# Optimization experiments

Hardware: AMD Instinct MI355X
Metric: run time of the kernel (lower is better)

## Reference

```python
import jax, jax.numpy as jnp
import numpy as np
from jax import lax

N_CLASS = 32000
N_HIDDEN = 512
S_ENC = 1024
S_DEC = 256


def setup_inputs() -> dict:
    key = jax.random.key(0)
    ks = jax.random.split(key, 16)
    C, H = N_CLASS, N_HIDDEN
    sC = np.float32(1.0 / np.sqrt(C))
    sH = np.float32(1.0 / np.sqrt(H))
    f32 = jnp.float32
    return {
        "encoder_inputs": jax.random.normal(ks[0], (1, S_ENC, C), f32),
        "hidden_0": jnp.zeros((1, 1, H), f32),
        "decoder_inputs": jax.random.normal(ks[1], (1, S_DEC, C), f32),
        # encoder RNN params (torch nn.RNN layout: W_ih [H,C], W_hh [H,H])
        "enc_Wih": jax.random.normal(ks[2], (H, C), f32) * sC,
        "enc_Whh": jax.random.normal(ks[3], (H, H), f32) * sH,
        "enc_bih": jax.random.normal(ks[4], (H,), f32) * sH,
        "enc_bhh": jax.random.normal(ks[5], (H,), f32) * sH,
        # decoder RNN params
        "dec_Wih": jax.random.normal(ks[6], (H, C), f32) * sC,
        "dec_Whh": jax.random.normal(ks[7], (H, H), f32) * sH,
        "dec_bih": jax.random.normal(ks[8], (H,), f32) * sH,
        "dec_bhh": jax.random.normal(ks[9], (H,), f32) * sH,
        # attention Linear [H,H]
        "attn_W": jax.random.normal(ks[10], (H, H), f32) * sH,
        "attn_b": jax.random.normal(ks[11], (H,), f32) * sH,
        # output Linear [C, 2H]
        "out_W": jax.random.normal(ks[12], (C, 2 * H), f32) * sH,
        "out_b": jax.random.normal(ks[13], (C,), f32) * sH,
    }


def _rnn_scan(x, h0, Wih, Whh, bih, bhh):
    # x: [S, C], h0: [H] -> hs: [S, H], hT: [H]  (tanh vanilla RNN)
    def step(h, xt):
        h = jnp.tanh(xt @ Wih.T + bih + h @ Whh.T + bhh)
        return h, h
    hT, hs = lax.scan(step, h0, x)
    return hs, hT


def reference(encoder_inputs, hidden_0, decoder_inputs,
              enc_Wih, enc_Whh, enc_bih, enc_bhh,
              dec_Wih, dec_Whh, dec_bih, dec_bhh,
              attn_W, attn_b, out_W, out_b):
    enc_x = encoder_inputs[0]   # [S_enc, C] (batch=1)
    dec_x = decoder_inputs[0]   # [S_dec, C]
    h0 = hidden_0[0, 0]         # [H]

    enc_hs, enc_hT = _rnn_scan(enc_x, h0, enc_Wih, enc_Whh, enc_bih, enc_bhh)

    # score_i = dot(dec_h, attn(enc_h_i)); precompute attn over all encoder states
    attn_enc = enc_hs @ attn_W.T + attn_b   # [S_enc, H]

    def dec_step(h, xt):
        h = jnp.tanh(xt @ dec_Wih.T + dec_bih + h @ dec_Whh.T + dec_bhh)  # [H]
        w = jax.nn.softmax(attn_enc @ h)      # [S_enc]
        context = w @ enc_hs                  # [H]
        out = jnp.concatenate([h, context]) @ out_W.T + out_b  # [C]
        return h, (out, w)

    _, (outputs, attn) = lax.scan(dec_step, enc_hT, dec_x)
    # outputs: [S_dec, n_class], attn: [S_dec, S_enc]
    return outputs, attn
```

## Files before the change

### kernel.cpp

```cpp
#include <hip/hip_runtime.h>

typedef _Float16 f16;
typedef _Float16 f16x2 __attribute__((ext_vector_type(2)));
typedef _Float16 f16x8 __attribute__((ext_vector_type(8)));
typedef float f32x4 __attribute__((ext_vector_type(4)));

#define NCLS 32000
#define NH   512
#define SE   1024
#define SD   256

static __device__ __forceinline__ f16x2 h2bc(unsigned int x) {
  return __builtin_bit_cast(f16x2, x);
}

static __device__ __forceinline__ float fdot2f(f16x2 a, f16x2 b, float c) {
#if __has_builtin(__builtin_amdgcn_fdot2)
  return __builtin_amdgcn_fdot2(a, b, c, false);
#else
  return c + (float)a[0]*(float)b[0] + (float)a[1]*(float)b[1];
#endif
}

static __device__ __forceinline__ uint4 gload16(const void* p) {
  uint4 r;
  asm volatile("global_load_dwordx4 %0, %1, off" : "=v"(r) : "v"(p));
  return r;
}
static __device__ __forceinline__ void waitvm0() {
  asm volatile("s_waitcnt vmcnt(0)" ::: "memory");
  __builtin_amdgcn_sched_barrier(0);
}

__global__ void k_cvt2(const float* __restrict__ s0, f16* __restrict__ d0,
                       const float* __restrict__ s1, f16* __restrict__ d1, int n) {
  int i = blockIdx.x*blockDim.x + threadIdx.x;
  int st = gridDim.x*blockDim.x;
  for (; i < 2*n; i += st) {
    if (i < n) d0[i] = (f16)s0[i];
    else       d1[i-n] = (f16)s1[i-n];
  }
}

template<int AF32, int BF32>
__global__ __launch_bounds__(1024, 4) void k_gemm6(
    const void* __restrict__ A0v, const void* __restrict__ B0v,
    f16* __restrict__ P0, float* __restrict__ C0, int M0, int gy0, int ldc0, int nb0,
    const void* __restrict__ A1v, const void* __restrict__ B1v,
    f16* __restrict__ P1, float* __restrict__ C1, int M1, int gy1, int ldc1,
    int gx, int lda, int ldb, const float* __restrict__ bias, int kLen)
{
  __shared__ f16 S[2][2][256][40];
  int tid = threadIdx.x;
  int lane = tid & 63;
  int wid = tid >> 6;
  int wr = wid >> 2, wc = wid & 3;

  int nwg = gridDim.x;
  int d = blockIdx.x;
  int q = nwg >> 3, rm = nwg & 7, xcd = d & 7, lin = d >> 3;
  int L = (xcd < rm ? xcd*(q+1) : rm*(q+1) + (xcd-rm)*q) + lin;

  const void* Av; const void* Bv; f16* P16; float* C32; int M, gy, ldc; int lid;
  if (L < nb0) { Av=A0v; Bv=B0v; P16=P0; C32=C0; M=M0; gy=gy0; ldc=ldc0; lid=L; }
  else { Av=A1v; Bv=B1v; P16=P1; C32=C1; M=M1; gy=gy1; ldc=ldc1; lid=L-nb0; }
  int gxy = gx*gy;
  int bz = lid / gxy; int rr2 = lid % gxy;
  int by = rr2 / gx, bx = rr2 % gx;

  long row0 = (long)by*256, col0 = (long)bx*256;
  long k0 = (long)bz*kLen;

  bool isA = tid < 512;
  int t2 = isA ? tid : tid - 512;
  int r = t2 >> 1, koff = (t2 & 1) * 16;

  const float* pf = nullptr; const f16* ph = nullptr;
  if (isA) {
    if constexpr (AF32) pf = (const float*)Av + (row0 + r)*(long)lda + k0 + koff;
    else                ph = (const f16*)Av  + (row0 + r)*(long)lda + k0 + koff;
  } else {
    if constexpr (BF32) pf = (const float*)Bv + (col0 + r)*(long)ldb + k0 + koff;
    else                ph = (const f16*)Bv  + (col0 + r)*(long)ldb + k0 + koff;
  }
  bool srcF = isA ? (AF32 != 0) : (BF32 != 0);

  f32x4 fa[4];
  uint4 ha[2];
  int nst = kLen >> 5;

#define G_LOAD(T) do { long gk = (long)(T)*32;                                  \
    if (srcF) { const f32x4* p = (const f32x4*)(pf + gk);                       \
      fa[0]=p[0]; fa[1]=p[1]; fa[2]=p[2]; fa[3]=p[3]; }                         \
    else { const uint4* p = (const uint4*)(ph + gk); ha[0]=p[0]; ha[1]=p[1]; }  \
  } while(0)

#define G_STORE(B) do {                                                         \
    f16* dst = &S[B][isA?0:1][r][koff];                                         \
    if (srcF) { f16x8 h0, h1;                                                   \
      _Pragma("unroll") for (int qq=0;qq<4;qq++){                               \
        h0[qq]=(f16)fa[0][qq]; h0[4+qq]=(f16)fa[1][qq];                         \
        h1[qq]=(f16)fa[2][qq]; h1[4+qq]=(f16)fa[3][qq]; }                       \
      *(f16x8*)dst = h0; *(f16x8*)(dst+8) = h1; }                               \
    else { *(uint4*)dst = ha[0]; *(uint4*)(dst+8) = ha[1]; }                    \
  } while(0)

  f32x4 acc[4][4];
  #pragma unroll
  for (int i=0;i<4;i++)
    #pragma unroll
    for (int j=0;j<4;j++)
      acc[i][j] = (f32x4){0.f,0.f,0.f,0.f};

  G_LOAD(0);
  G_STORE(0);
  __syncthreads();

  int cur = 0;
  for (int t = 0; t < nst; ++t) {
    if (t+1 < nst) G_LOAD(t+1);

    f16x8 a[4], b[4];
    #pragma unroll
    for (int i=0;i<4;i++)
      a[i] = *(const f16x8*)&S[cur][0][wr*64 + i*16 + (lane&15)][(lane>>4)*8];
    #pragma unroll
    for (int j=0;j<4;j++)
      b[j] = *(const f16x8*)&S[cur][1][wc*64 + j*16 + (lane&15)][(lane>>4)*8];
    #pragma unroll
    for (int i=0;i<4;i++)
      #pragma unroll
      for (int j=0;j<4;j++)
        acc[i][j] = __builtin_amdgcn_mfma_f32_16x16x32_f16(a[i], b[j], acc[i][j], 0,0,0);

    if (t+1 < nst) G_STORE(cur^1);
    __syncthreads();
    cur ^= 1;
  }

  if (P16) {
    long base = (long)bz * M;
    #pragma unroll
    for (int i=0;i<4;i++)
      #pragma unroll
      for (int j=0;j<4;j++)
        #pragma unroll
        for (int v=0;v<4;v++) {
          long row = row0 + wr*64 + i*16 + ((lane>>4)*4) + v;
          long col = col0 + wc*64 + j*16 + (lane&15);
          P16[(base + row)*(long)ldc + col] = (f16)acc[i][j][v];
        }
  } else {
    #pragma unroll
    for (int i=0;i<4;i++)
      #pragma unroll
      for (int j=0;j<4;j++)
        #pragma unroll
        for (int v=0;v<4;v++) {
          long row = row0 + wr*64 + i*16 + ((lane>>4)*4) + v;
          long col = col0 + wc*64 + j*16 + (lane&15);
          float val = acc[i][j][v];
          if (bias) val += bias[col];
          C32[row*(long)ldc + col] = val;
        }
  }
#undef G_LOAD
#undef G_STORE
}

__global__ __launch_bounds__(512, 4) void k_gemm7(
    const f16* __restrict__ A16, int lda, const float* __restrict__ B32, int ldb,
    float* __restrict__ C32, int ldc, const float* __restrict__ bias, int kLen)
{
  __shared__ f16 SA[2][256][40];
  __shared__ f16 SB[2][64][40];
  int tid = threadIdx.x;
  int lane = tid & 63;
  int wid = tid >> 6;
  int wr = wid >> 1, wc = wid & 1;

  int nwg = gridDim.x, d = blockIdx.x;
  int q = nwg >> 3, rm = nwg & 7, xcd = d & 7, lin = d >> 3;
  int L = (xcd < rm ? xcd*(q+1) : rm*(q+1) + (xcd-rm)*q) + lin;
  long col0 = (long)L * 64;

  int ra0 = tid >> 2,        ka0 = (tid & 3) * 8;
  int ra1 = (tid+512) >> 2,  ka1 = ((tid+512) & 3) * 8;
  int rb  = tid >> 3,        kb  = (tid & 7) * 4;

  const f16*   pA0 = A16 + (long)ra0*lda + ka0;
  const f16*   pA1 = A16 + (long)ra1*lda + ka1;
  const float* pB  = B32 + (col0 + rb)*(long)ldb + kb;

  uint4 ha0, ha1; f32x4 fb;
  int nst = kLen >> 5;

#define G_LOAD(T) do { long gk = (long)(T)*32;                                  \
    ha0 = *(const uint4*)(pA0 + gk);                                            \
    ha1 = *(const uint4*)(pA1 + gk);                                            \
    fb  = *(const f32x4*)(pB + gk);                                             \
  } while(0)

#define G_STORE(Bf) do {                                                        \
    *(uint4*)&SA[Bf][ra0][ka0] = ha0;                                           \
    *(uint4*)&SA[Bf][ra1][ka1] = ha1;                                           \
    f16x2 h0; h0[0]=(f16)fb[0]; h0[1]=(f16)fb[1];                               \
    f16x2 h1; h1[0]=(f16)fb[2]; h1[1]=(f16)fb[3];                               \
    *(f16x2*)&SB[Bf][rb][kb] = h0;                                              \
    *(f16x2*)&SB[Bf][rb][kb+2] = h1;                                            \
  } while(0)

  f32x4 acc[4][2];
  #pragma unroll
  for (int i=0;i<4;i++)
    #pragma unroll
    for (int j=0;j<2;j++)
      acc[i][j] = (f32x4){0.f,0.f,0.f,0.f};

  G_LOAD(0);
  G_STORE(0);
  __syncthreads();

  int cur = 0;
  for (int t = 0; t < nst; ++t) {
    if (t+1 < nst) G_LOAD(t+1);

    f16x8 a[4], b[2];
    #pragma unroll
    for (int i=0;i<4;i++)
      a[i] = *(const f16x8*)&SA[cur][wr*64 + i*16 + (lane&15)][(lane>>4)*8];
    #pragma unroll
    for (int j=0;j<2;j++)
      b[j] = *(const f16x8*)&SB[cur][wc*32 + j*16 + (lane&15)][(lane>>4)*8];
    #pragma unroll
    for (int i=0;i<4;i++)
      #pragma unroll
      for (int j=0;j<2;j++)
        acc[i][j] = __builtin_amdgcn_mfma_f32_16x16x32_f16(a[i], b[j], acc[i][j], 0,0,0);

    if (t+1 < nst) G_STORE(cur^1);
    __syncthreads();
    cur ^= 1;
  }

  #pragma unroll
  for (int i=0;i<4;i++)
    #pragma unroll
    for (int j=0;j<2;j++)
      #pragma unroll
      for (int v=0;v<4;v++) {
        long row = wr*64 + i*16 + ((lane>>4)*4) + v;
        long col = col0 + wc*32 + j*16 + (lane&15);
        C32[row*(long)ldc + col] = acc[i][j][v] + bias[col];
      }
#undef G_LOAD
#undef G_STORE
}

template<int AF32, int BF32>
__global__ __launch_bounds__(256, 4) void k_gemm3(
    const void* __restrict__ Av, int lda, const void* __restrict__ Bv, int ldb,
    float* __restrict__ C32, f16* __restrict__ C16, int ldc,
    const float* __restrict__ bias, int M, int kLen)
{
  __shared__ f16 At[2][64][72];
  __shared__ f16 Bt[2][64][72];
  int tid = threadIdx.x;
  int lane = tid & 63;
  int wid = tid >> 6;
  int wr = wid >> 1, wc = wid & 1;

  int gx = gridDim.x, gy = gridDim.y;
  int d = blockIdx.x + gx*(blockIdx.y + gy*blockIdx.z);
  int nwg = gx*gy*gridDim.z;
  int q = nwg >> 3, rm = nwg & 7, xcd = d & 7, lin = d >> 3;
  int L = (xcd < rm ? xcd*(q+1) : rm*(q+1) + (xcd-rm)*q) + lin;
  int bx = L % gx; int rem = L / gx;
  int by = rem % gy; int bz = rem / gy;

  long row0 = (long)by*64, col0 = (long)bx*64;
  long k0 = (long)bz*kLen;

  const float* A32 = (const float*)Av; const f16* A16 = (const f16*)Av;
  const float* B32 = (const float*)Bv; const f16* B16 = (const f16*)Bv;

  int r = tid >> 2, koff = (tid & 3) * 16;

  const float* pAf = A32 + (row0 + r)*(long)lda + k0 + koff;
  const float* pBf = B32 + (col0 + r)*(long)ldb + k0 + koff;
  const f16*   pAh = A16 + (row0 + r)*(long)lda + k0 + koff;
  const f16*   pBh = B16 + (col0 + r)*(long)ldb + k0 + koff;

  f32x4 fa[4], fb[4];
  uint4 ha[2], hb[2];

  int nst = kLen >> 6;

#define G_LOAD(T) do { long gk = (long)(T)*64;                                  \
    if constexpr (AF32) { const f32x4* p = (const f32x4*)(pAf + gk);            \
      fa[0]=p[0]; fa[1]=p[1]; fa[2]=p[2]; fa[3]=p[3]; }                         \
    else { const uint4* p = (const uint4*)(pAh + gk); ha[0]=p[0]; ha[1]=p[1]; } \
    if constexpr (BF32) { const f32x4* p = (const f32x4*)(pBf + gk);            \
      fb[0]=p[0]; fb[1]=p[1]; fb[2]=p[2]; fb[3]=p[3]; }                         \
    else { const uint4* p = (const uint4*)(pBh + gk); hb[0]=p[0]; hb[1]=p[1]; } \
  } while(0)

#define G_STORE(B) do {                                                         \
    if constexpr (AF32) { f16x8 h0, h1;                                         \
      _Pragma("unroll") for (int qq=0;qq<4;qq++){                               \
        h0[qq]=(f16)fa[0][qq]; h0[4+qq]=(f16)fa[1][qq];                         \
        h1[qq]=(f16)fa[2][qq]; h1[4+qq]=(f16)fa[3][qq]; }                       \
      *(f16x8*)&At[B][r][koff] = h0; *(f16x8*)&At[B][r][koff+8] = h1; }         \
    else { *(uint4*)&At[B][r][koff] = ha[0]; *(uint4*)&At[B][r][koff+8] = ha[1]; } \
    if constexpr (BF32) { f16x8 h2, h3;                                         \
      _Pragma("unroll") for (int qq=0;qq<4;qq++){                               \
        h2[qq]=(f16)fb[0][qq]; h2[4+qq]=(f16)fb[1][qq];                         \
        h3[qq]=(f16)fb[2][qq]; h3[4+qq]=(f16)fb[3][qq]; }                       \
      *(f16x8*)&Bt[B][r][koff] = h2; *(f16x8*)&Bt[B][r][koff+8] = h3; }         \
    else { *(uint4*)&Bt[B][r][koff] = hb[0]; *(uint4*)&Bt[B][r][koff+8] = hb[1]; } \
  } while(0)

  f32x4 acc[2][2];
  #pragma unroll
  for (int i=0;i<2;i++)
    #pragma unroll
    for (int j=0;j<2;j++)
      acc[i][j] = (f32x4){0.f,0.f,0.f,0.f};

  G_LOAD(0);
  G_STORE(0);
  __syncthreads();

  int cur = 0;
  for (int t = 0; t < nst; ++t) {
    if (t+1 < nst) G_LOAD(t+1);

    f16x8 a[2][2], b[2][2];
    #pragma unroll
    for (int kk=0;kk<2;kk++) {
      #pragma unroll
      for (int i=0;i<2;i++)
        a[kk][i] = *(const f16x8*)&At[cur][wr*32 + i*16 + (lane&15)][kk*32 + (lane>>4)*8];
      #pragma unroll
      for (int j=0;j<2;j++)
        b[kk][j] = *(const f16x8*)&Bt[cur][wc*32 + j*16 + (lane&15)][kk*32 + (lane>>4)*8];
    }
    #pragma unroll
    for (int kk=0;kk<2;kk++)
      #pragma unroll
      for (int i=0;i<2;i++)
        #pragma unroll
        for (int j=0;j<2;j++)
          acc[i][j] = __builtin_amdgcn_mfma_f32_16x16x32_f16(a[kk][i], b[kk][j], acc[i][j], 0,0,0);

    if (t+1 < nst) G_STORE(cur^1);
    __syncthreads();
    cur ^= 1;
  }

  long zofs = (long)bz * (long)M * (long)ldc;
  #pragma unroll
  for (int i=0;i<2;i++)
    #pragma unroll
    for (int j=0;j<2;j++)
      #pragma unroll
      for (int v=0;v<4;v++) {
        long row = row0 + wr*32 + i*16 + ((lane>>4)*4) + v;
        long col = col0 + wc*32 + j*16 + (lane&15);
        float val = acc[i][j][v];
        if (bias) val += bias[col];
        if (C32) C32[zofs + row*(long)ldc + col] = val;
        else     C16[row*(long)ldc + col] = (f16)val;
      }
#undef G_LOAD
#undef G_STORE
}

__global__ void k_reduceh2(
    const f16* __restrict__ pE, float* __restrict__ oE,
    const float* __restrict__ be1, const float* __restrict__ be2, int MNe,
    const f16* __restrict__ pD, float* __restrict__ oD,
    const float* __restrict__ bd1, const float* __restrict__ bd2, int MNd,
    int S, int nbE)
{
  const f16* part; float* out; const float* b1; const float* b2; int MN, i;
  if ((int)blockIdx.x < nbE) {
    part = pE; out = oE; b1 = be1; b2 = be2; MN = MNe;
    i = (blockIdx.x*256 + threadIdx.x)*4;
  } else {
    part = pD; out = oD; b1 = bd1; b2 = bd2; MN = MNd;
    i = ((blockIdx.x-nbE)*256 + threadIdx.x)*4;
  }
  if (i >= MN) return;
  float s0=0.f, s1=0.f, s2=0.f, s3=0.f;
  for (int z = 0; z < S; ++z) {
    uint2 v = *(const uint2*)(part + (long)z*MN + i);
    f16x2 lo = h2bc(v.x), hi = h2bc(v.y);
    s0 += (float)lo[0]; s1 += (float)lo[1];
    s2 += (float)hi[0]; s3 += (float)hi[1];
  }
  out[i+0] = s0 + b1[(i+0)&511] + b2[(i+0)&511];
  out[i+1] = s1 + b1[(i+1)&511] + b2[(i+1)&511];
  out[i+2] = s2 + b1[(i+2)&511] + b2[(i+2)&511];
  out[i+3] = s3 + b1[(i+3)&511] + b2[(i+3)&511];
}

__global__ void k_reduce16(const float* __restrict__ part, f16* __restrict__ out,
                           int ld, int S, int MN, int N) {
  int i = blockIdx.x*256 + threadIdx.x;
  if (i >= MN) return;
  float s = 0.f;
  for (int z = 0; z < S; ++z) s += part[(long)z*MN + i];
  out[(long)(i / N)*ld + (i % N)] = (f16)s;
}

__global__ __launch_bounds__(256) void k_gemm_f32(
    const float* __restrict__ A, int lda,
    const float* __restrict__ B, const float* __restrict__ B2,
    const float* __restrict__ bk, int ldb,
    float* __restrict__ C, int ldc, int kLen, int M)
{
  __shared__ float As[64][33], Bs[64][33];
  int tid = threadIdx.x;
  int r0 = blockIdx.x*64, c0 = blockIdx.y*64;
  long zk = (long)blockIdx.z * kLen;
  int ty = tid >> 4, tx = tid & 15;
  float acc[4][4];
  #pragma unroll
  for (int i=0;i<4;i++)
    #pragma unroll
    for (int j=0;j<4;j++) acc[i][j] = 0.f;
  int sr = tid >> 2, skq = (tid & 3) * 8;
  for (int k0 = 0; k0 < kLen; k0 += 32) {
    __syncthreads();
    long ao = (long)(r0+sr)*lda + zk + k0 + skq;
    long bo = (long)(c0+sr)*ldb + zk + k0 + skq;
    float4 a0 = *(const float4*)&A[ao];
    float4 a1 = *(const float4*)&A[ao + 4];
    float4 b0 = *(const float4*)&B[bo];
    float4 b1 = *(const float4*)&B[bo + 4];
    if (B2) {
      float4 c0v = *(const float4*)&B2[bo];
      float4 c1v = *(const float4*)&B2[bo + 4];
      float4 k0v = *(const float4*)&bk[zk + k0 + skq];
      float4 k1v = *(const float4*)&bk[zk + k0 + skq + 4];
      b0.x += c0v.x + k0v.x; b0.y += c0v.y + k0v.y;
      b0.z += c0v.z + k0v.z; b0.w += c0v.w + k0v.w;
      b1.x += c1v.x + k1v.x; b1.y += c1v.y + k1v.y;
      b1.z += c1v.z + k1v.z; b1.w += c1v.w + k1v.w;
    }
    As[sr][skq+0]=a0.x; As[sr][skq+1]=a0.y; As[sr][skq+2]=a0.z; As[sr][skq+3]=a0.w;
    As[sr][skq+4]=a1.x; As[sr][skq+5]=a1.y; As[sr][skq+6]=a1.z; As[sr][skq+7]=a1.w;
    Bs[sr][skq+0]=b0.x; Bs[sr][skq+1]=b0.y; Bs[sr][skq+2]=b0.z; Bs[sr][skq+3]=b0.w;
    Bs[sr][skq+4]=b1.x; Bs[sr][skq+5]=b1.y; Bs[sr][skq+6]=b1.z; Bs[sr][skq+7]=b1.w;
    __syncthreads();
    #pragma unroll
    for (int k=0;k<32;k++) {
      float av[4], bv[4];
      #pragma unroll
      for (int i=0;i<4;i++) av[i] = As[ty*4+i][k];
      #pragma unroll
      for (int j=0;j<4;j++) bv[j] = Bs[tx*4+j][k];
      #pragma unroll
      for (int i=0;i<4;i++)
        #pragma unroll
        for (int j=0;j<4;j++) acc[i][j] += av[i]*bv[j];
    }
  }
  long zofs = (long)blockIdx.z * (long)M * (long)ldc;
  #pragma unroll
  for (int i=0;i<4;i++)
    #pragma unroll
    for (int j=0;j<4;j++) {
      int row = r0 + ty*4 + i, col = c0 + tx*4 + j;
      C[zofs + (long)row*ldc + col] = acc[i][j];
    }
}

__global__ __launch_bounds__(512, 1) void k_scan3(
    const float* __restrict__ encpre,
    const float* __restrict__ decpre,
    const f16* __restrict__ WE, const f16* __restrict__ WD,
    const float* __restrict__ seed,
    float* __restrict__ ehs32, f16* __restrict__ ehsT, int ldT,
    float* __restrict__ dhs32, f16* __restrict__ dA, int ldA,
    int GE, int CH, int WARM)
{
  __shared__ uint4 wl[2][8][512];
  __shared__ f16 hbuf[2][512];
  int tid = threadIdx.x;
  int rj = tid & 7, ri = tid >> 3;

  uint4 wv[6][8];

#define LOADW(Wp) do { const f16* _wb = (Wp);                                   \
    _Pragma("unroll") for (int rr=0; rr<6; ++rr)                                \
      _Pragma("unroll") for (int jb=0; jb<8; ++jb)                              \
        wv[rr][jb] = gload16(_wb + ((ri*8+rr)*512 + rj*64 + jb*8));             \
    _Pragma("unroll") for (int rr=0; rr<2; ++rr)                                \
      _Pragma("unroll") for (int jb=0; jb<8; ++jb)                              \
        wl[rr][jb][tid] =                                                       \
            *(const uint4*)(_wb + ((ri*8+6+rr)*512 + rj*64 + jb*8));            \
  } while(0)

  int g = blockIdx.x;
  long uout = (g < GE) ? (long)g*CH : 1024 + (long)(g-GE)*CH;
  long uend = uout + CH;
  long u0 = uout - WARM; if (u0 < 0) u0 = 0;

  LOADW(u0 < 1024 ? WE : WD);

  {
    float h0v = seed[tid];
    int b = tid >> 3, w = tid & 7;
    int pb = ((b&7)<<3) | (b>>3);
    hbuf[0][pb*8 + w] = (f16)h0v;
  }
  waitvm0();
  __syncthreads();

  int cur = 0;

  auto step = [&](const float* __restrict__ prerow, int isenc, long u) {
    float pv = prerow[tid];
    const f16* hb = hbuf[cur];
    float acc[8] = {0.f,0.f,0.f,0.f,0.f,0.f,0.f,0.f};
    #pragma unroll
    for (int jb=0; jb<8; ++jb) {
      uint4 hv = *(const uint4*)(hb + (((jb<<3)|rj)<<3));
      f16x2 hp0 = h2bc(hv.x), hp1 = h2bc(hv.y), hp2 = h2bc(hv.z), hp3 = h2bc(hv.w);
      #pragma unroll
      for (int rr=0; rr<6; ++rr) {
        uint4 wp = wv[rr][jb];
        acc[rr] = fdot2f(h2bc(wp.x), hp0, acc[rr]);
        acc[rr] = fdot2f(h2bc(wp.y), hp1, acc[rr]);
        acc[rr] = fdot2f(h2bc(wp.z), hp2, acc[rr]);
        acc[rr] = fdot2f(h2bc(wp.w), hp3, acc[rr]);
      }
      uint4 w6 = wl[0][jb][tid];
      acc[6] = fdot2f(h2bc(w6.x), hp0, acc[6]);
      acc[6] = fdot2f(h2bc(w6.y), hp1, acc[6]);
      acc[6] = fdot2f(h2bc(w6.z), hp2, acc[6]);
      acc[6] = fdot2f(h2bc(w6.w), hp3, acc[6]);
      uint4 w7 = wl[1][jb][tid];
      acc[7] = fdot2f(h2bc(w7.x), hp0, acc[7]);
      acc[7] = fdot2f(h2bc(w7.y), hp1, acc[7]);
      acc[7] = fdot2f(h2bc(w7.z), hp2, acc[7]);
      acc[7] = fdot2f(h2bc(w7.w), hp3, acc[7]);
    }
    int b2 = rj & 4, b1 = rj & 2, b0 = rj & 1;
    float t4[4];
    #pragma unroll
    for (int k=0;k<4;k++) {
      float keep = b2 ? acc[4+k] : acc[k];
      float send = b2 ? acc[k]   : acc[4+k];
      t4[k] = keep + __shfl_xor(send, 4);
    }
    float t2[2];
    #pragma unroll
    for (int k=0;k<2;k++) {
      float keep = b1 ? t4[2+k] : t4[k];
      float send = b1 ? t4[k]   : t4[2+k];
      t2[k] = keep + __shfl_xor(send, 2);
    }
    float keep = b0 ? t2[1] : t2[0];
    float send = b0 ? t2[0] : t2[1];
    float tot = keep + __shfl_xor(send, 1);

    float s = tot + pv;
    float ex = __expf(2.f*s);
    float h = 1.f - 2.f/(ex + 1.f);

    {
      int b = tid >> 3, w = tid & 7;
      int pb = ((b&7)<<3) | (b>>3);
      hbuf[cur^1][pb*8 + w] = (f16)h;
    }
    if (u >= uout) {
      if (isenc) {
        ehs32[u*512 + tid] = h;
        ehsT[(long)tid*ldT + u] = (f16)h;
      } else {
        long td = u - 1024;
        dhs32[td*512 + tid] = h;
        dA[td*(long)ldA + tid] = (f16)h;
      }
    }
    cur ^= 1;
    __syncthreads();
  };

  long u = u0;
  long e1 = uend < 1024 ? uend : 1024;
  for (; u < e1; ++u) step(encpre + u*512, 1, u);
  if (u < uend && u0 < 1024) {
    LOADW(WD);
    waitvm0();
    __syncthreads();
  }
  for (; u < uend; ++u) step(decpre + (u-1024)*512, 0, u);
#undef LOADW
}

__global__ __launch_bounds__(256) void k_softmax(const float* __restrict__ SP,
    float* __restrict__ outw, f16* __restrict__ probs, int S)
{
  int row = blockIdx.x, tid = threadIdx.x;
  int lane = tid & 63, wid = tid >> 6;
  __shared__ float red[4];
  float v[4];
  #pragma unroll
  for (int k=0;k<4;k++) {
    long o = (long)row*1024 + tid + k*256;
    float s = 0.f;
    for (int z = 0; z < S; ++z) s += SP[(long)z*256*1024 + o];
    v[k] = s;
  }
  float m = fmaxf(fmaxf(v[0],v[1]), fmaxf(v[2],v[3]));
  #pragma unroll
  for (int d=32; d; d>>=1) m = fmaxf(m, __shfl_xor(m, d));
  if (lane==0) red[wid] = m;
  __syncthreads();
  m = fmaxf(fmaxf(red[0],red[1]), fmaxf(red[2],red[3]));
  float e[4], s = 0.f;
  #pragma unroll
  for (int k=0;k<4;k++) { e[k] = __expf(v[k]-m); s += e[k]; }
  #pragma unroll
  for (int d=32; d; d>>=1) s += __shfl_xor(s, d);
  __syncthreads();
  if (lane==0) red[wid] = s;
  __syncthreads();
  s = red[0]+red[1]+red[2]+red[3];
  float inv = 1.f/s;
  #pragma unroll
  for (int k=0;k<4;k++) {
    int c = tid + k*256;
    float w = e[k]*inv;
    outw[(long)row*1024 + c] = w;
    probs[(long)row*1024 + c] = (f16)w;
  }
}

extern "C" void kernel_launch(void* const* d_in, const int* in_sizes, int n_in,
                              void* d_out, int out_size, void* d_ws, size_t ws_size,
                              hipStream_t stream) {
  const float* enc_x = (const float*)d_in[0];
  const float* h0    = (const float*)d_in[1];
  const float* dec_x = (const float*)d_in[2];
  const float* eWih  = (const float*)d_in[3];
  const float* eWhh  = (const float*)d_in[4];
  const float* ebih  = (const float*)d_in[5];
  const float* ebhh  = (const float*)d_in[6];
  const float* dWih  = (const float*)d_in[7];
  const float* dWhh  = (const float*)d_in[8];
  const float* dbih  = (const float*)d_in[9];
  const float* dbhh  = (const float*)d_in[10];
  const float* aW    = (const float*)d_in[11];
  const float* ab    = (const float*)d_in[12];
  const float* oW    = (const float*)d_in[13];
  const float* ob    = (const float*)d_in[14];

  float* out0 = (float*)d_out;
  float* out1 = out0 + (size_t)SD*NCLS;

  f16* o_partE = (f16*)out0;
  f16* o_partD = (f16*)((char*)d_out + 26214400);

  char* ws = (char*)d_ws;
  f16*   o_concatA16 = (f16*)  (ws + 0);
  char*  A           = ws + 524288;
  float* o_encpre    = (float*)(A + 0);
  float* o_decpre    = (float*)(A + 2097152);
  f16*   o_WhhE      = (f16*)  (A + 2621440);
  f16*   o_WhhD      = (f16*)  (A + 3145728);
  float* o_enchs32   = (float*)(A + 3670016);
  f16*   o_enchsT16  = (f16*)  (A + 5767168);
  float* o_dechs32   = (float*)(A + 8912896);
  f16*   o_probs16   = (f16*)  (A + 10485760);
  float* o_ctxpart   = (float*)(A + 11010048);
  float* o_aepart    = (float*)(A + 13107200);
  float* o_scpart    = (float*)(A + 17301504);

  k_cvt2<<<1024,256,0,stream>>>(eWhh, o_WhhE, dWhh, o_WhhD, 512*512);

  k_gemm6<1,1><<<250,1024,0,stream>>>(
      enc_x, eWih, o_partE, nullptr, 1024, 4, 512, 200,
      dec_x, dWih, o_partD, nullptr, 256, 1, 512,
      2, NCLS, NCLS, nullptr, 1280);
  k_reduceh2<<<640,256,0,stream>>>(
      o_partE, o_encpre, ebih, ebhh, 1024*512,
      o_partD, o_decpre, dbih, dbhh, 256*512, 25, 512);

  k_scan3<<<160,512,0,stream>>>(o_encpre, o_decpre, o_WhhE, o_WhhD, h0,
      o_enchs32, o_enchsT16, 1024,
      o_dechs32, o_concatA16, 1024,
      128, 8, 32);

  k_gemm_f32<<<dim3(16,8,2),256,0,stream>>>(o_enchs32, 512,
      aW, nullptr, nullptr, 512, o_aepart, 512, 256, 1024);

  k_gemm_f32<<<dim3(4,16,4),256,0,stream>>>(o_dechs32, 512,
      o_aepart, o_aepart + (size_t)1024*512, ab, 512, o_scpart, 1024, 128, 256);

  k_softmax<<<256,256,0,stream>>>(o_scpart, out1, o_probs16, 4);

  k_gemm3<0,0><<<dim3(8,4,4),256,0,stream>>>(o_probs16, 1024, o_enchsT16, 1024,
      o_ctxpart, nullptr, 512, nullptr, 256, 256);
  k_reduce16<<<512,256,0,stream>>>(o_ctxpart, o_concatA16 + 512, 1024, 4, 256*512, 512);

  k_gemm7<<<500,512,0,stream>>>(o_concatA16, 1024, oW, 1024,
      out0, NCLS, ob, 1024);
}
```

Baseline: 313.7 us.

## Reassociate attention scores via transposed attn_W and deepen split-K partitioning

The attention score path no longer projects all 1024 encoder states through attn_W. It first computes v = dec_hs @ attn_W (a 256x512 product, using a transposed copy made in the prep kernel) and then scores = v @ enc_hs^T. This drops the attn_b term, which is constant across encoder positions and cancels in the softmax. The input-projection GEMM now uses 400 workgroups with a smaller K chunk (800), so there are more split-K partials; the encoder partials are spread across two buffers and the reduce is adjusted to match. The context GEMM also moves from 4 to 8 K splits. The extra partial traffic and reduction work are the cost paid for more parallelism, and the workspace layout is reshuffled with aliased buffers.

```diff
diff --git a/kernel.cpp b/kernel.cpp
--- a/kernel.cpp
+++ b/kernel.cpp
@@ -32,23 +32,31 @@
   __builtin_amdgcn_sched_barrier(0);
 }
 
-__global__ void k_cvt2(const float* __restrict__ s0, f16* __restrict__ d0,
-                       const float* __restrict__ s1, f16* __restrict__ d1, int n) {
+__global__ void k_prep(const float* __restrict__ eW, f16* __restrict__ dE,
+                       const float* __restrict__ dW, f16* __restrict__ dD,
+                       const float* __restrict__ aW, float* __restrict__ Wt,
+                       int n) {
   int i = blockIdx.x*blockDim.x + threadIdx.x;
   int st = gridDim.x*blockDim.x;
-  for (; i < 2*n; i += st) {
-    if (i < n) d0[i] = (f16)s0[i];
-    else       d1[i-n] = (f16)s1[i-n];
+  for (; i < 3*n; i += st) {
+    if (i < n)        dE[i] = (f16)eW[i];
+    else if (i < 2*n) dD[i-n] = (f16)dW[i-n];
+    else {
+      int j = i - 2*n;
+      int m = j >> 9, k = j & 511;
+      Wt[j] = aW[(k << 9) | m];
+    }
   }
 }
 
 template<int AF32, int BF32>
 __global__ __launch_bounds__(1024, 4) void k_gemm6(
     const void* __restrict__ A0v, const void* __restrict__ B0v,
-    f16* __restrict__ P0, float* __restrict__ C0, int M0, int gy0, int ldc0, int nb0,
+    f16* __restrict__ P0a, f16* __restrict__ P0b, int zsp0,
+    int M0, int gy0, int ldc0, int nb0,
     const void* __restrict__ A1v, const void* __restrict__ B1v,
-    f16* __restrict__ P1, float* __restrict__ C1, int M1, int gy1, int ldc1,
-    int gx, int lda, int ldb, const float* __restrict__ bias, int kLen)
+    f16* __restrict__ P1, int M1, int gy1, int ldc1,
+    int gx, int lda, int ldb, int kLen)
 {
   __shared__ f16 S[2][2][256][40];
   int tid = threadIdx.x;
@@ -61,9 +69,9 @@
   int q = nwg >> 3, rm = nwg & 7, xcd = d & 7, lin = d >> 3;
   int L = (xcd < rm ? xcd*(q+1) : rm*(q+1) + (xcd-rm)*q) + lin;
 
-  const void* Av; const void* Bv; f16* P16; float* C32; int M, gy, ldc; int lid;
-  if (L < nb0) { Av=A0v; Bv=B0v; P16=P0; C32=C0; M=M0; gy=gy0; ldc=ldc0; lid=L; }
-  else { Av=A1v; Bv=B1v; P16=P1; C32=C1; M=M1; gy=gy1; ldc=ldc1; lid=L-nb0; }
+  const void* Av; const void* Bv; int M, gy, ldc; int lid; bool job0;
+  if (L < nb0) { Av=A0v; Bv=B0v; M=M0; gy=gy0; ldc=ldc0; lid=L; job0=true; }
+  else { Av=A1v; Bv=B1v; M=M1; gy=gy1; ldc=ldc1; lid=L-nb0; job0=false; }
   int gxy = gx*gy;
   int bz = lid / gxy; int rr2 = lid % gxy;
   int by = rr2 / gx, bx = rr2 % gx;
@@ -138,32 +146,20 @@
     cur ^= 1;
   }
 
-  if (P16) {
-    long base = (long)bz * M;
-    #pragma unroll
-    for (int i=0;i<4;i++)
-      #pragma unroll
-      for (int j=0;j<4;j++)
-        #pragma unroll
-        for (int v=0;v<4;v++) {
-          long row = row0 + wr*64 + i*16 + ((lane>>4)*4) + v;
-          long col = col0 + wc*64 + j*16 + (lane&15);
-          P16[(base + row)*(long)ldc + col] = (f16)acc[i][j][v];
-        }
-  } else {
-    #pragma unroll
-    for (int i=0;i<4;i++)
-      #pragma unroll
-      for (int j=0;j<4;j++)
-        #pragma unroll
-        for (int v=0;v<4;v++) {
-          long row = row0 + wr*64 + i*16 + ((lane>>4)*4) + v;
-          long col = col0 + wc*64 + j*16 + (lane&15);
-          float val = acc[i][j][v];
-          if (bias) val += bias[col];
-          C32[row*(long)ldc + col] = val;
-        }
-  }
+  f16* Pb; long zz;
+  if (job0) { if (bz < zsp0) { Pb = P0a; zz = bz; } else { Pb = P0b; zz = bz - zsp0; } }
+  else { Pb = P1; zz = bz; }
+  long base = zz * (long)M;
+  #pragma unroll
+  for (int i=0;i<4;i++)
+    #pragma unroll
+    for (int j=0;j<4;j++)
+      #pragma unroll
+      for (int v=0;v<4;v++) {
+        long row = row0 + wr*64 + i*16 + ((lane>>4)*4) + v;
+        long col = col0 + wc*64 + j*16 + (lane&15);
+        Pb[(base + row)*(long)ldc + col] = (f16)acc[i][j][v];
+      }
 #undef G_LOAD
 #undef G_STORE
 }
@@ -377,28 +373,30 @@
 }
 
 __global__ void k_reduceh2(
-    const f16* __restrict__ pE, float* __restrict__ oE,
+    const f16* __restrict__ pEa, const f16* __restrict__ pEb, int SEa, int SEb,
+    float* __restrict__ oE,
     const float* __restrict__ be1, const float* __restrict__ be2, int MNe,
-    const f16* __restrict__ pD, float* __restrict__ oD,
+    const f16* __restrict__ pD, int SD_, float* __restrict__ oD,
     const float* __restrict__ bd1, const float* __restrict__ bd2, int MNd,
-    int S, int nbE)
+    int nbE)
 {
-  const f16* part; float* out; const float* b1; const float* b2; int MN, i;
-  if ((int)blockIdx.x < nbE) {
-    part = pE; out = oE; b1 = be1; b2 = be2; MN = MNe;
-    i = (blockIdx.x*256 + threadIdx.x)*4;
-  } else {
-    part = pD; out = oD; b1 = bd1; b2 = bd2; MN = MNd;
-    i = ((blockIdx.x-nbE)*256 + threadIdx.x)*4;
-  }
+  bool isE = (int)blockIdx.x < nbE;
+  int i = isE ? (blockIdx.x*256 + threadIdx.x)*4
+              : ((blockIdx.x-nbE)*256 + threadIdx.x)*4;
+  int MN = isE ? MNe : MNd;
   if (i >= MN) return;
   float s0=0.f, s1=0.f, s2=0.f, s3=0.f;
-  for (int z = 0; z < S; ++z) {
-    uint2 v = *(const uint2*)(part + (long)z*MN + i);
-    f16x2 lo = h2bc(v.x), hi = h2bc(v.y);
-    s0 += (float)lo[0]; s1 += (float)lo[1];
-    s2 += (float)hi[0]; s3 += (float)hi[1];
-  }
+#define ACC(P,S) for (int z = 0; z < (S); ++z) {                                \
+    uint2 v = *(const uint2*)((P) + (long)z*MN + i);                            \
+    f16x2 lo = h2bc(v.x), hi = h2bc(v.y);                                       \
+    s0 += (float)lo[0]; s1 += (float)lo[1];                                     \
+    s2 += (float)hi[0]; s3 += (float)hi[1]; }
+  if (isE) { ACC(pEa, SEa); ACC(pEb, SEb); }
+  else     { ACC(pD, SD_); }
+#undef ACC
+  const float* b1 = isE ? be1 : bd1;
+  const float* b2 = isE ? be2 : bd2;
+  float* out = isE ? oE : oD;
   out[i+0] = s0 + b1[(i+0)&511] + b2[(i+0)&511];
   out[i+1] = s1 + b1[(i+1)&511] + b2[(i+1)&511];
   out[i+2] = s2 + b1[(i+2)&511] + b2[(i+2)&511];
@@ -415,9 +413,7 @@
 }
 
 __global__ __launch_bounds__(256) void k_gemm_f32(
-    const float* __restrict__ A, int lda,
-    const float* __restrict__ B, const float* __restrict__ B2,
-    const float* __restrict__ bk, int ldb,
+    const float* __restrict__ A, int lda, const float* __restrict__ B, int ldb,
     float* __restrict__ C, int ldc, int kLen, int M)
 {
   __shared__ float As[64][33], Bs[64][33];
@@ -439,16 +435,6 @@
     float4 a1 = *(const float4*)&A[ao + 4];
     float4 b0 = *(const float4*)&B[bo];
     float4 b1 = *(const float4*)&B[bo + 4];
-    if (B2) {
-      float4 c0v = *(const float4*)&B2[bo];
-      float4 c1v = *(const float4*)&B2[bo + 4];
-      float4 k0v = *(const float4*)&bk[zk + k0 + skq];
-      float4 k1v = *(const float4*)&bk[zk + k0 + skq + 4];
-      b0.x += c0v.x + k0v.x; b0.y += c0v.y + k0v.y;
-      b0.z += c0v.z + k0v.z; b0.w += c0v.w + k0v.w;
-      b1.x += c1v.x + k1v.x; b1.y += c1v.y + k1v.y;
-      b1.z += c1v.z + k1v.z; b1.w += c1v.w + k1v.w;
-    }
     As[sr][skq+0]=a0.x; As[sr][skq+1]=a0.y; As[sr][skq+2]=a0.z; As[sr][skq+3]=a0.w;
     As[sr][skq+4]=a1.x; As[sr][skq+5]=a1.y; As[sr][skq+6]=a1.z; As[sr][skq+7]=a1.w;
     Bs[sr][skq+0]=b0.x; Bs[sr][skq+1]=b0.y; Bs[sr][skq+2]=b0.z; Bs[sr][skq+3]=b0.w;
@@ -656,57 +642,58 @@
   const float* dbih  = (const float*)d_in[9];
   const float* dbhh  = (const float*)d_in[10];
   const float* aW    = (const float*)d_in[11];
-  const float* ab    = (const float*)d_in[12];
   const float* oW    = (const float*)d_in[13];
   const float* ob    = (const float*)d_in[14];
 
   float* out0 = (float*)d_out;
   float* out1 = out0 + (size_t)SD*NCLS;
 
-  f16* o_partE = (f16*)out0;
-  f16* o_partD = (f16*)((char*)d_out + 26214400);
+  f16* o_partEa = (f16*)d_out;
 
   char* ws = (char*)d_ws;
   f16*   o_concatA16 = (f16*)  (ws + 0);
-  char*  A           = ws + 524288;
-  float* o_encpre    = (float*)(A + 0);
-  float* o_decpre    = (float*)(A + 2097152);
-  f16*   o_WhhE      = (f16*)  (A + 2621440);
-  f16*   o_WhhD      = (f16*)  (A + 3145728);
-  float* o_enchs32   = (float*)(A + 3670016);
-  f16*   o_enchsT16  = (f16*)  (A + 5767168);
-  float* o_dechs32   = (float*)(A + 8912896);
-  f16*   o_probs16   = (f16*)  (A + 10485760);
-  float* o_ctxpart   = (float*)(A + 11010048);
-  float* o_aepart    = (float*)(A + 13107200);
-  float* o_scpart    = (float*)(A + 17301504);
-
-  k_cvt2<<<1024,256,0,stream>>>(eWhh, o_WhhE, dWhh, o_WhhD, 512*512);
-
-  k_gemm6<1,1><<<250,1024,0,stream>>>(
-      enc_x, eWih, o_partE, nullptr, 1024, 4, 512, 200,
-      dec_x, dWih, o_partD, nullptr, 256, 1, 512,
-      2, NCLS, NCLS, nullptr, 1280);
+  f16*   o_WhhE      = (f16*)  (ws + 524288);
+  f16*   o_WhhD      = (f16*)  (ws + 1048576);
+  float* o_Wt        = (float*)(ws + 1572864);
+  char*  B           = ws + 2621440;
+  f16*   o_partEb    = (f16*)  (B + 0);
+  f16*   o_partD     = (f16*)  (B + 8388608);
+  float* o_encpre    = (float*)(B + 18874368);
+  float* o_decpre    = (float*)(B + 20971520);
+  float* o_enchs32   = (float*)(B + 0);
+  f16*   o_enchsT16  = (f16*)  (B + 2097152);
+  float* o_dechs32   = (float*)(B + 3145728);
+  float* o_v32       = (float*)(B + 3670016);
+  f16*   o_probs16   = (f16*)  (B + 4194304);
+  float* o_scpart    = (float*)(B + 4718592);
+  float* o_ctxpart   = (float*)(B + 8912896);
+
+  k_prep<<<1024,256,0,stream>>>(eWhh, o_WhhE, dWhh, o_WhhD, aW, o_Wt, 512*512);
+
+  k_gemm6<1,1><<<400,1024,0,stream>>>(
+      enc_x, eWih, o_partEa, o_partEb, 32, 1024, 4, 512, 320,
+      dec_x, dWih, o_partD, 256, 1, 512,
+      2, NCLS, NCLS, 800);
   k_reduceh2<<<640,256,0,stream>>>(
-      o_partE, o_encpre, ebih, ebhh, 1024*512,
-      o_partD, o_decpre, dbih, dbhh, 256*512, 25, 512);
+      o_partEa, o_partEb, 32, 8, o_encpre, ebih, ebhh, 1024*512,
+      o_partD, 40, o_decpre, dbih, dbhh, 256*512, 512);
 
   k_scan3<<<160,512,0,stream>>>(o_encpre, o_decpre, o_WhhE, o_WhhD, h0,
       o_enchs32, o_enchsT16, 1024,
       o_dechs32, o_concatA16, 1024,
       128, 8, 32);
 
-  k_gemm_f32<<<dim3(16,8,2),256,0,stream>>>(o_enchs32, 512,
-      aW, nullptr, nullptr, 512, o_aepart, 512, 256, 1024);
-
-  k_gemm_f32<<<dim3(4,16,4),256,0,stream>>>(o_dechs32, 512,
-      o_aepart, o_aepart + (size_t)1024*512, ab, 512, o_scpart, 1024, 128, 256);
+  k_gemm_f32<<<dim3(4,8,1),256,0,stream>>>(o_dechs32, 512, o_Wt, 512,
+      o_v32, 512, 512, 256);
+
+  k_gemm_f32<<<dim3(4,16,4),256,0,stream>>>(o_v32, 512, o_enchs32, 512,
+      o_scpart, 1024, 128, 256);
 
   k_softmax<<<256,256,0,stream>>>(o_scpart, out1, o_probs16, 4);
 
-  k_gemm3<0,0><<<dim3(8,4,4),256,0,stream>>>(o_probs16, 1024, o_enchsT16, 1024,
-      o_ctxpart, nullptr, 512, nullptr, 256, 256);
-  k_reduce16<<<512,256,0,stream>>>(o_ctxpart, o_concatA16 + 512, 1024, 4, 256*512, 512);
+  k_gemm3<0,0><<<dim3(8,4,8),256,0,stream>>>(o_probs16, 1024, o_enchsT16, 1024,
+      o_ctxpart, nullptr, 512, nullptr, 256, 128);
+  k_reduce16<<<512,256,0,stream>>>(o_ctxpart, o_concatA16 + 512, 1024, 8, 256*512, 512);
 
   k_gemm7<<<500,512,0,stream>>>(o_concatA16, 1024, oW, 1024,
       out0, NCLS, ob, 1024);
```

New measurement: 348.8 us. 11.2% more time.
